# Kernel tuning notes

Hardware: AMD Instinct MI355X
Metric: run time of the kernel (lower is better)

The kernel has to match this reference:

```python
import jax, jax.numpy as jnp
import numpy as np

# dims: episodes E, steps S, comm length L, hidden H, rnn input IN, comm vocab OUT
E, S, L, H, IN, OUT = 64, 32, 32, 1024, 2048, 64
TAU = 2.0      # MTRNN leaky-integrator time constant
EPS = 1e-5     # BatchNorm eps


def setup_inputs() -> dict:
    key = jax.random.key(0)
    ks = jax.random.split(key, 16)
    def p(k, shape, scale=0.02):
        return jax.random.normal(k, shape, jnp.float32) * scale
    return {
        "h_w_action": jax.random.normal(ks[0], (E, S, IN), jnp.float32),
        # MTRNN cell
        "Wx": p(ks[1], (IN, H)), "bx": jnp.zeros((H,), jnp.float32),
        "Wh": p(ks[2], (H, H)), "bh": jnp.zeros((H,), jnp.float32),
        # Ted_Conv1d: 4 branches, kernels 1/3/5/7, each H//4 out channels (OIH layout)
        "w1": p(ks[3], (H // 4, H, 1)), "b1": jnp.zeros((H // 4,), jnp.float32),
        "w3": p(ks[4], (H // 4, H, 3)), "b3": jnp.zeros((H // 4,), jnp.float32),
        "w5": p(ks[5], (H // 4, H, 5)), "b5": jnp.zeros((H // 4,), jnp.float32),
        "w7": p(ks[6], (H // 4, H, 7)), "b7": jnp.zeros((H // 4,), jnp.float32),
        # BatchNorm1d affine
        "gamma": jnp.ones((H,), jnp.float32), "beta": jnp.zeros((H,), jnp.float32),
        # PReLU (single shared slope, torch default init 0.25)
        "prelu_a": jnp.array(0.25, jnp.float32),
        # output Linear
        "Wout": p(ks[7], (H, OUT)), "bout": jnp.zeros((OUT,), jnp.float32),
    }


def _conv(x, w, b):
    # x: [N, C, L], w: [O, I, k], 'same' padding for odd kernels
    pad = (w.shape[-1] - 1) // 2
    y = jax.lax.conv_general_dilated(x, w, (1,), [(pad, pad)],
                                     dimension_numbers=('NCH', 'OIH', 'NCH'))
    return y + b[None, :, None]


def reference(h_w_action, Wx, bx, Wh, bh, w1, b1, w3, b3, w5, b5, w7, b7,
              gamma, beta, prelu_a, Wout, bout):
    # MTRNN: same input every step; leaky integration h' = (1-1/tau)h + (1/tau)tanh(Wx x + Wh h)
    x_r = h_w_action @ Wx + bx                      # [E,S,H], constant across steps
    h0 = jnp.zeros((E, S, H), h_w_action.dtype)

    def step(h, _):
        h_new = (1.0 - 1.0 / TAU) * h + (1.0 / TAU) * jnp.tanh(x_r + h @ Wh + bh)
        return h_new, h_new

    _, hs = jax.lax.scan(step, h0, None, length=L)  # [L,E,S,H]
    hs = hs.transpose(1, 2, 0, 3).reshape(E * S, L, H)

    # multi-kernel conv over the comm-length axis
    xc = hs.transpose(0, 2, 1)                      # [N,H,L]
    y = jnp.concatenate([_conv(xc, w1, b1), _conv(xc, w3, b3),
                         _conv(xc, w5, b5), _conv(xc, w7, b7)], axis=1)  # [N,H,L]

    # BatchNorm1d (training-mode batch stats over N and L), affine
    mean = y.mean(axis=(0, 2), keepdims=True)
    var = y.var(axis=(0, 2), keepdims=True)
    y = (y - mean) * jax.lax.rsqrt(var + EPS) * gamma[None, :, None] + beta[None, :, None]

    # PReLU; Dropout is identity at eval
    y = jnp.where(y > 0, y, prelu_a * y)

    y = y.transpose(0, 2, 1).reshape(E, S, L, H)
    return y @ Wout + bout                          # [E,S,L,OUT]
```

## Files before the change

### kernel.cpp

```cpp
#include <hip/hip_runtime.h>
#include <cstdint>
#include <cmath>

#define DI __device__ __forceinline__


typedef __attribute__((ext_vector_type(8))) short bf16x8;
typedef __attribute__((ext_vector_type(4))) short s16x4;
typedef __attribute__((ext_vector_type(4))) float f32x4;

DI float bf2f(short u){
  union { unsigned int i; float f; } v; v.i = ((unsigned int)(unsigned short)u) << 16; return v.f;
}
DI short f2bf(float f){
  unsigned int x = __builtin_bit_cast(unsigned int, f);
  unsigned int r = (x + 0x7FFFu + ((x >> 16) & 1u)) >> 16;
  return (short)(unsigned short)r;
}
DI void gload16(const void* g, void* l){
  __builtin_amdgcn_global_load_lds(
      (const __attribute__((address_space(1))) unsigned int*)g,
      (__attribute__((address_space(3))) unsigned int*)l, 16, 0, 0);
}

template<int BM, int BN, int MODE>
__global__ __launch_bounds__(256)
void gemm_k(const short* __restrict__ A, long lda,
            const short* __restrict__ Bt, long ldb, int Ksteps,
            const float* __restrict__ bias,
            float* __restrict__ f32out,
            const float* __restrict__ f32in,
            short* __restrict__ bfout, int jj)
{
  constexpr int WTM = BM / 2, WTN = BN / 2;
  constexpr int FM = WTM / 16, FN = WTN / 16;
  constexpr int AIT = BM / 32, BIT = BN / 32;
  __shared__ short As[BM * 64];
  __shared__ short Bs[BN * 64];
  const int tid = threadIdx.x;
  const int w = tid >> 6, l = tid & 63;
  const int wr = w >> 1, wc = w & 1;
  const int lr = l & 15, lk = (l >> 4) << 3;
  const int brow = blockIdx.x * BM;
  const int bcol = blockIdx.y * BN;

  int coff = 0, jout = 0;
  bool first = false;
  if constexpr (MODE == 2) {
    const int bb = bcol >> 7;
    const int dlt = (bb < 2) ? -3 : (bb < 6) ? -2 : (bb < 12) ? -1
                  : (bb < 20) ? 0 : (bb < 26) ? 1 : (bb < 30) ? 2 : 3;
    coff = (dlt == -3) ? 768 : (dlt == -2) ? 256 : (dlt == -1) ? -512
         : (dlt == 0) ? -1536 : (dlt == 1) ? -2304 : (dlt == 2) ? -2816 : -3072;
    jout = jj - dlt;
    if (jout < 0 || jout > 31) return;
    const int ubranch = (bcol + coff) >> 8;
    first = (dlt == -(ubranch < jout ? ubranch : jout));
  }

  f32x4 acc[FM][FN];
  #pragma unroll
  for (int i = 0; i < FM; i++)
    #pragma unroll
    for (int j = 0; j < FN; j++) {
      acc[i][j][0] = 0.f; acc[i][j][1] = 0.f; acc[i][j][2] = 0.f; acc[i][j][3] = 0.f;
    }

  const int rsub = tid >> 3;
  const int koff = (tid & 7) << 3;
  const short* ap[AIT];
  const short* bp[BIT];
  #pragma unroll
  for (int it = 0; it < AIT; ++it)
    ap[it] = A + (long)(brow + it * 32 + rsub) * lda + koff;
  #pragma unroll
  for (int it = 0; it < BIT; ++it)
    bp[it] = Bt + (long)(bcol + it * 32 + rsub) * ldb + koff;

  for (int ks = 0; ks < Ksteps; ++ks) {
    #pragma unroll
    for (int it = 0; it < AIT; ++it) {
      gload16(ap[it], As + ((it * 256 + (w << 6)) << 3));
      ap[it] += 64;
    }
    #pragma unroll
    for (int it = 0; it < BIT; ++it) {
      gload16(bp[it], Bs + ((it * 256 + (w << 6)) << 3));
      bp[it] += 64;
    }
    __syncthreads();
    #pragma unroll
    for (int kk = 0; kk < 64; kk += 32) {
      bf16x8 a[FM], b[FN];
      #pragma unroll
      for (int i = 0; i < FM; i++)
        a[i] = *(const bf16x8*)&As[(wr * WTM + i * 16 + lr) * 64 + kk + lk];
      #pragma unroll
      for (int j = 0; j < FN; j++)
        b[j] = *(const bf16x8*)&Bs[(wc * WTN + j * 16 + lr) * 64 + kk + lk];
      #pragma unroll
      for (int i = 0; i < FM; i++)
        #pragma unroll
        for (int j = 0; j < FN; j++)
          acc[i][j] = __builtin_amdgcn_mfma_f32_16x16x32_bf16(a[i], b[j], acc[i][j], 0, 0, 0);
    }
    __syncthreads();
  }

  const int rbase = brow + wr * WTM;
  const int cbase = bcol + wc * WTN;
  const int rl = (l >> 4) << 2;
  #pragma unroll
  for (int i = 0; i < FM; i++) {
    #pragma unroll
    for (int j = 0; j < FN; j++) {
      #pragma unroll
      for (int r = 0; r < 4; r++) {
        const int row = rbase + i * 16 + rl + r;
        const int col = cbase + j * 16 + lr;
        const float v = acc[i][j][r];
        if constexpr (MODE == 0) {
          f32out[(long)row * 1024 + col] = v + bias[col];
        } else if constexpr (MODE == 1) {
          const long idx = (long)row * 1024 + col;
          const float hp = bf2f(A[(long)row * lda + col]);
          const float hn = 0.5f * hp + 0.5f * tanhf(f32in[idx] + v + bias[col]);
          bfout[idx] = f2bf(hn);
        } else if constexpr (MODE == 2) {
          short* yp = bfout + ((long)row * 32 + jout) * 1024 + (col + coff);
          if (first) *yp = f2bf(v);
          else       *yp = f2bf(bf2f(*yp) + v);
        }
      }
    }
  }
}

__global__ __launch_bounds__(256)
void g5_bn(const short* __restrict__ y, const short* __restrict__ WoutT,
           const float* __restrict__ scal, const float* __restrict__ shft,
           const float* __restrict__ aP, const float* __restrict__ bout,
           float* __restrict__ out)
{
  __shared__ short As[128 * 64];
  __shared__ short Bs[64 * 64];
  __shared__ float sS[1024], sB[1024];
  const int tid = threadIdx.x;
  const int w = tid >> 6, l = tid & 63;
  const int wr = w >> 1, wc = w & 1;
  const int lr = l & 15, lk = (l >> 4) << 3;
  const int m0 = blockIdx.x * 128;
  for (int i = tid; i < 1024; i += 256) { sS[i] = scal[i]; sB[i] = shft[i]; }
  const float a = *aP;
  __syncthreads();

  f32x4 acc[4][2];
  #pragma unroll
  for (int i = 0; i < 4; i++)
    #pragma unroll
    for (int j = 0; j < 2; j++) {
      acc[i][j][0] = 0.f; acc[i][j][1] = 0.f; acc[i][j][2] = 0.f; acc[i][j][3] = 0.f;
    }

  const int rsub = tid >> 3;
  const int koff = (tid & 7) << 3;
  const short* yp[4];
  #pragma unroll
  for (int it = 0; it < 4; ++it)
    yp[it] = y + (long)(m0 + it * 32 + rsub) * 1024 + koff;
  const short* bp[2];
  #pragma unroll
  for (int it = 0; it < 2; ++it)
    bp[it] = WoutT + (long)(it * 32 + rsub) * 1024 + koff;

  for (int ks = 0; ks < 16; ++ks) {
    #pragma unroll
    for (int it = 0; it < 2; ++it) {
      gload16(bp[it], Bs + ((it * 256 + (w << 6)) << 3));
      bp[it] += 64;
    }
    const int c0 = ks * 64 + koff;
    #pragma unroll
    for (int it = 0; it < 4; ++it) {
      bf16x8 v = *(const bf16x8*)yp[it];
      yp[it] += 64;
      #pragma unroll
      for (int e = 0; e < 8; ++e) {
        float f = bf2f(v[e]) * sS[c0 + e] + sB[c0 + e];
        v[e] = f2bf(f > 0.f ? f : a * f);
      }
      *(bf16x8*)(As + ((it * 256 + tid) << 3)) = v;
    }
    __syncthreads();
    #pragma unroll
    for (int kk = 0; kk < 64; kk += 32) {
      bf16x8 af[4], bf_[2];
      #pragma unroll
      for (int i = 0; i < 4; i++)
        af[i] = *(const bf16x8*)&As[(wr * 64 + i * 16 + lr) * 64 + kk + lk];
      #pragma unroll
      for (int j = 0; j < 2; j++)
        bf_[j] = *(const bf16x8*)&Bs[(wc * 32 + j * 16 + lr) * 64 + kk + lk];
      #pragma unroll
      for (int i = 0; i < 4; i++)
        #pragma unroll
        for (int j = 0; j < 2; j++)
          acc[i][j] = __builtin_amdgcn_mfma_f32_16x16x32_bf16(af[i], bf_[j], acc[i][j], 0, 0, 0);
    }
    __syncthreads();
  }

  const int rbase = m0 + wr * 64, cbase = wc * 32;
  const int rl = (l >> 4) << 2;
  #pragma unroll
  for (int i = 0; i < 4; i++)
    #pragma unroll
    for (int j = 0; j < 2; j++)
      #pragma unroll
      for (int r = 0; r < 4; r++) {
        const int row = rbase + i * 16 + rl + r;
        const int col = cbase + j * 16 + lr;
        out[(long)row * 64 + col] = acc[i][j][r] + bout[col];
      }
}

__global__ void zero16(float4* __restrict__ p, long n)
{
  long i = (long)blockIdx.x * 256 + threadIdx.x;
  if (i < n) p[i] = float4{0.f, 0.f, 0.f, 0.f};
}

__global__ void cvt4_f32_bf16(const float* __restrict__ in, short* __restrict__ out, int n4)
{
  int i = blockIdx.x * 256 + threadIdx.x;
  if (i >= n4) return;
  float4 v = ((const float4*)in)[i];
  s16x4 o; o[0] = f2bf(v.x); o[1] = f2bf(v.y); o[2] = f2bf(v.z); o[3] = f2bf(v.w);
  ((s16x4*)out)[i] = o;
}

__global__ void transpose_f32_bf16(const float* __restrict__ in, short* __restrict__ out,
                                   int R, int C)
{
  __shared__ short tile[32][33];
  const int tx = threadIdx.x & 31, ty = threadIdx.x >> 5;
  const int c0 = blockIdx.x * 32, r0 = blockIdx.y * 32;
  #pragma unroll
  for (int i = 0; i < 32; i += 8)
    tile[ty + i][tx] = f2bf(in[(long)(r0 + ty + i) * C + (c0 + tx)]);
  __syncthreads();
  #pragma unroll
  for (int i = 0; i < 32; i += 8)
    out[(long)(c0 + ty + i) * R + (r0 + tx)] = tile[tx][ty + i];
}

__global__ void build_wpack(const float* __restrict__ w1, const float* __restrict__ w3,
                            const float* __restrict__ w5, const float* __restrict__ w7,
                            short* __restrict__ Wp)
{
  const int pc = blockIdx.x;
  int dlt, c;
  if      (pc < 256)  { dlt = -3; c = pc + 768; }
  else if (pc < 768)  { dlt = -2; c = pc + 256; }
  else if (pc < 1536) { dlt = -1; c = pc - 512; }
  else if (pc < 2560) { dlt = 0;  c = pc - 1536; }
  else if (pc < 3328) { dlt = 1;  c = pc - 2304; }
  else if (pc < 3840) { dlt = 2;  c = pc - 2816; }
  else                { dlt = 3;  c = pc - 3072; }
  const int b = c >> 8, kb = 2 * b + 1, t = dlt + b, oo = c & 255;
  const float* w = (b == 0) ? w1 : (b == 1) ? w3 : (b == 2) ? w5 : w7;
  short* dst = Wp + (long)pc * 1024;
  for (int i = threadIdx.x; i < 1024; i += 256)
    dst[i] = f2bf(w[((long)oo * 1024 + i) * kb + t]);
}

__global__ void bn_stats1(const short* __restrict__ y, float* __restrict__ psum,
                          float* __restrict__ pssq)
{
  const int c0 = threadIdx.x * 4;
  float s0 = 0, s1 = 0, s2 = 0, s3 = 0, q0 = 0, q1 = 0, q2 = 0, q3 = 0;
  const long base = (long)blockIdx.x * 64;
  for (int r = 0; r < 64; ++r) {
    s16x4 v = *(const s16x4*)(y + (base + r) * 1024 + c0);
    float f0 = bf2f(v[0]), f1 = bf2f(v[1]), f2v = bf2f(v[2]), f3 = bf2f(v[3]);
    s0 += f0; s1 += f1; s2 += f2v; s3 += f3;
    q0 += f0 * f0; q1 += f1 * f1; q2 += f2v * f2v; q3 += f3 * f3;
  }
  ((float4*)(psum + (long)blockIdx.x * 1024))[threadIdx.x] = float4{s0, s1, s2, s3};
  ((float4*)(pssq + (long)blockIdx.x * 1024))[threadIdx.x] = float4{q0, q1, q2, q3};
}

__global__ __launch_bounds__(256)
void bn_stats2(const float* __restrict__ psum, const float* __restrict__ pssq,
               const float* __restrict__ gamma, const float* __restrict__ beta,
               float* __restrict__ scale, float* __restrict__ shift)
{
  __shared__ float reds[256], redq[256];
  const int ch = threadIdx.x & 7;
  const int rseg = threadIdx.x >> 3;
  const int c = blockIdx.x * 8 + ch;
  float s = 0.f, q = 0.f;
  #pragma unroll 4
  for (int k = 0; k < 32; ++k) {
    const long row = rseg + 32 * k;
    s += psum[row * 1024 + c];
    q += pssq[row * 1024 + c];
  }
  reds[rseg * 8 + ch] = s;
  redq[rseg * 8 + ch] = q;
  __syncthreads();
  #pragma unroll
  for (int st = 16; st > 0; st >>= 1) {
    if (rseg < st) {
      reds[rseg * 8 + ch] += reds[(rseg + st) * 8 + ch];
      redq[rseg * 8 + ch] += redq[(rseg + st) * 8 + ch];
    }
    __syncthreads();
  }
  if (rseg == 0) {
    const float inv = 1.f / 65536.f;
    float mean = reds[ch] * inv;
    float var = redq[ch] * inv - mean * mean;
    float sc = gamma[c] * rsqrtf(var + 1e-5f);
    scale[c] = sc;
    shift[c] = beta[c] - mean * sc;
  }
}

extern "C" void kernel_launch(void* const* d_in, const int* in_sizes, int n_in,
                              void* d_out, int out_size, void* d_ws, size_t ws_size,
                              hipStream_t stream)
{
  const float* h_w_action = (const float*)d_in[0];
  const float* Wx   = (const float*)d_in[1];
  const float* bx   = (const float*)d_in[2];
  const float* Wh   = (const float*)d_in[3];
  const float* bh   = (const float*)d_in[4];
  const float* w1   = (const float*)d_in[5];
  const float* w3   = (const float*)d_in[7];
  const float* w5   = (const float*)d_in[9];
  const float* w7   = (const float*)d_in[11];
  const float* gamma = (const float*)d_in[13];
  const float* beta  = (const float*)d_in[14];
  const float* prelu = (const float*)d_in[15];
  const float* Wout  = (const float*)d_in[16];
  const float* bout  = (const float*)d_in[17];
  float* out = (float*)d_out;

  char* p = (char*)d_ws;
  auto alloc = [&](size_t bytes) -> char* {
    char* r = p; p += (bytes + 255) & ~(size_t)255; return r;
  };
  short* y     = (short*)alloc(65536L * 1024 * 2);
  float* xr    = (float*)alloc(2048L * 1024 * 4);
  float* psum  = (float*)alloc(1024L * 1024 * 4);
  float* pssq  = (float*)alloc(1024L * 1024 * 4);
  short* hb0   = (short*)alloc(2048L * 1024 * 2);
  short* hb1   = (short*)alloc(2048L * 1024 * 2);
  short* A1    = (short*)alloc(2048L * 2048 * 2);
  short* WxT   = (short*)alloc(1024L * 2048 * 2);
  short* WhT   = (short*)alloc(1024L * 1024 * 2);
  short* Wp    = (short*)alloc(4096L * 1024 * 2);
  short* WoutT = (short*)alloc(64L * 1024 * 2);
  float* scal  = (float*)alloc(1024 * 4);
  float* shft  = (float*)alloc(1024 * 4);

  if ((size_t)(p - (char*)d_ws) > ws_size) return;

  zero16<<<1024, 256, 0, stream>>>((float4*)hb0, 2048L * 1024 * 2 / 16);

  cvt4_f32_bf16<<<4096, 256, 0, stream>>>(h_w_action, A1, 2048 * 2048 / 4);
  transpose_f32_bf16<<<dim3(32, 64), 256, 0, stream>>>(Wx, WxT, 2048, 1024);
  transpose_f32_bf16<<<dim3(32, 32), 256, 0, stream>>>(Wh, WhT, 1024, 1024);
  transpose_f32_bf16<<<dim3(2, 32), 256, 0, stream>>>(Wout, WoutT, 1024, 64);
  build_wpack<<<4096, 256, 0, stream>>>(w1, w3, w5, w7, Wp);

  gemm_k<64, 64, 0><<<dim3(32, 16), 256, 0, stream>>>(
      A1, 2048, WxT, 2048, 32, bx, xr, nullptr, nullptr, 0);

  short* hb[2] = {hb0, hb1};
  for (int s = 1; s <= 32; ++s) {
    gemm_k<64, 64, 1><<<dim3(32, 16), 256, 0, stream>>>(
        hb[(s - 1) & 1], 1024, WhT, 1024, 16, bh, nullptr, xr, hb[s & 1], 0);
    gemm_k<128, 128, 2><<<dim3(16, 32), 256, 0, stream>>>(
        hb[s & 1], 1024, Wp, 1024, 16, nullptr, nullptr, nullptr, y, s - 1);
  }

  bn_stats1<<<1024, 256, 0, stream>>>(y, psum, pssq);
  bn_stats2<<<128, 256, 0, stream>>>(psum, pssq, gamma, beta, scal, shft);

  g5_bn<<<dim3(512, 1), 256, 0, stream>>>(y, WoutT, scal, shft, prelu, bout, out);
}
```

Before: 2.046 ms.

## Store recurrent states in padded buffer and run conv as one batched GEMM

The RNN steps now write each hidden state straight into a zero-padded per-sequence buffer (38 slots). The 32 per-step scatter/accumulate conv GEMMs are replaced by a single large GEMM after the recurrence. That GEMM reads shifted windows of the padded states and loops only over the taps each 256-column branch needs. This removes 32 small launches and the read-modify-write bf16 accumulation into y, in exchange for a larger workspace and a workspace-size-dependent fallback path.

```diff
diff --git a/kernel.cpp b/kernel.cpp
--- a/kernel.cpp
+++ b/kernel.cpp
@@ -30,7 +30,7 @@
             const float* __restrict__ bias,
             float* __restrict__ f32out,
             const float* __restrict__ f32in,
-            short* __restrict__ bfout, int jj)
+            short* __restrict__ bfout, long ldout, int jj)
 {
   constexpr int WTM = BM / 2, WTN = BN / 2;
   constexpr int FM = WTM / 16, FN = WTN / 16;
@@ -41,8 +41,8 @@
   const int w = tid >> 6, l = tid & 63;
   const int wr = w >> 1, wc = w & 1;
   const int lr = l & 15, lk = (l >> 4) << 3;
-  const int brow = blockIdx.x * BM;
-  const int bcol = blockIdx.y * BN;
+  const int brow = (MODE == 4) ? blockIdx.y * BM : blockIdx.x * BM;
+  const int bcol = (MODE == 4) ? blockIdx.x * BN : blockIdx.y * BN;
 
   int coff = 0, jout = 0;
   bool first = false;
@@ -68,27 +68,8 @@
 
   const int rsub = tid >> 3;
   const int koff = (tid & 7) << 3;
-  const short* ap[AIT];
-  const short* bp[BIT];
-  #pragma unroll
-  for (int it = 0; it < AIT; ++it)
-    ap[it] = A + (long)(brow + it * 32 + rsub) * lda + koff;
-  #pragma unroll
-  for (int it = 0; it < BIT; ++it)
-    bp[it] = Bt + (long)(bcol + it * 32 + rsub) * ldb + koff;
-
-  for (int ks = 0; ks < Ksteps; ++ks) {
-    #pragma unroll
-    for (int it = 0; it < AIT; ++it) {
-      gload16(ap[it], As + ((it * 256 + (w << 6)) << 3));
-      ap[it] += 64;
-    }
-    #pragma unroll
-    for (int it = 0; it < BIT; ++it) {
-      gload16(bp[it], Bs + ((it * 256 + (w << 6)) << 3));
-      bp[it] += 64;
-    }
-    __syncthreads();
+
+  auto compute = [&]() {
     #pragma unroll
     for (int kk = 0; kk < 64; kk += 32) {
       bf16x8 a[FM], b[FN];
@@ -104,7 +85,62 @@
         for (int j = 0; j < FN; j++)
           acc[i][j] = __builtin_amdgcn_mfma_f32_16x16x32_bf16(a[i], b[j], acc[i][j], 0, 0, 0);
     }
-    __syncthreads();
+  };
+
+  if constexpr (MODE == 4) {
+    const int b = bcol >> 8;
+    const int d0 = 3 - b, d1 = 3 + b;
+    const short* ap[AIT];
+    #pragma unroll
+    for (int it = 0; it < AIT; ++it) {
+      const int m = brow + it * 32 + rsub;
+      ap[it] = A + ((long)(m >> 5) * 38 + (m & 31) + d0) * 1024 + koff;
+    }
+    for (int d = d0; d <= d1; ++d) {
+      const short* bp[BIT];
+      #pragma unroll
+      for (int it = 0; it < BIT; ++it)
+        bp[it] = Bt + (long)(d * 1024 + bcol + it * 32 + rsub) * 1024 + koff;
+      for (int ks = 0; ks < 16; ++ks) {
+        #pragma unroll
+        for (int it = 0; it < AIT; ++it) {
+          gload16(ap[it], As + ((it * 256 + (w << 6)) << 3));
+          ap[it] += 64;
+        }
+        #pragma unroll
+        for (int it = 0; it < BIT; ++it) {
+          gload16(bp[it], Bs + ((it * 256 + (w << 6)) << 3));
+          bp[it] += 64;
+        }
+        __syncthreads();
+        compute();
+        __syncthreads();
+      }
+    }
+  } else {
+    const short* ap[AIT];
+    const short* bp[BIT];
+    #pragma unroll
+    for (int it = 0; it < AIT; ++it)
+      ap[it] = A + (long)(brow + it * 32 + rsub) * lda + koff;
+    #pragma unroll
+    for (int it = 0; it < BIT; ++it)
+      bp[it] = Bt + (long)(bcol + it * 32 + rsub) * ldb + koff;
+    for (int ks = 0; ks < Ksteps; ++ks) {
+      #pragma unroll
+      for (int it = 0; it < AIT; ++it) {
+        gload16(ap[it], As + ((it * 256 + (w << 6)) << 3));
+        ap[it] += 64;
+      }
+      #pragma unroll
+      for (int it = 0; it < BIT; ++it) {
+        gload16(bp[it], Bs + ((it * 256 + (w << 6)) << 3));
+        bp[it] += 64;
+      }
+      __syncthreads();
+      compute();
+      __syncthreads();
+    }
   }
 
   const int rbase = brow + wr * WTM;
@@ -122,14 +158,15 @@
         if constexpr (MODE == 0) {
           f32out[(long)row * 1024 + col] = v + bias[col];
         } else if constexpr (MODE == 1) {
-          const long idx = (long)row * 1024 + col;
           const float hp = bf2f(A[(long)row * lda + col]);
-          const float hn = 0.5f * hp + 0.5f * tanhf(f32in[idx] + v + bias[col]);
-          bfout[idx] = f2bf(hn);
+          const float hn = 0.5f * hp + 0.5f * tanhf(f32in[(long)row * 1024 + col] + v + bias[col]);
+          bfout[(long)row * ldout + col] = f2bf(hn);
         } else if constexpr (MODE == 2) {
           short* yp = bfout + ((long)row * 32 + jout) * 1024 + (col + coff);
           if (first) *yp = f2bf(v);
           else       *yp = f2bf(bf2f(*yp) + v);
+        } else if constexpr (MODE == 4) {
+          bfout[(long)row * 1024 + col] = f2bf(v);
         }
       }
     }
@@ -230,6 +267,16 @@
   if (i < n) p[i] = float4{0.f, 0.f, 0.f, 0.f};
 }
 
+__global__ void zpad(short* __restrict__ hsPad)
+{
+  long i = (long)blockIdx.x * 256 + threadIdx.x;
+  const long n = i / (6 * 128);
+  const int rem = (int)(i % (6 * 128));
+  const int sl = rem >> 7, c16 = rem & 127;
+  const int slot = sl < 3 ? sl : sl + 32;
+  ((float4*)(hsPad + (n * 38 + slot) * 1024))[c16] = float4{0.f, 0.f, 0.f, 0.f};
+}
+
 __global__ void cvt4_f32_bf16(const float* __restrict__ in, short* __restrict__ out, int n4)
 {
   int i = blockIdx.x * 256 + threadIdx.x;
@@ -252,6 +299,23 @@
   #pragma unroll
   for (int i = 0; i < 32; i += 8)
     out[(long)(c0 + ty + i) * R + (r0 + tx)] = tile[tx][ty + i];
+}
+
+__global__ void build_convw(const float* __restrict__ w1, const float* __restrict__ w3,
+                            const float* __restrict__ w5, const float* __restrict__ w7,
+                            short* __restrict__ WtT)
+{
+  const int doid = blockIdx.x;
+  const int d = doid >> 10, o = doid & 1023;
+  const int b = o >> 8, k = 2 * b + 1, t = d - 3 + b, oo = o & 255;
+  const float* w = (b == 0) ? w1 : (b == 1) ? w3 : (b == 2) ? w5 : w7;
+  short* dst = WtT + (long)doid * 1024;
+  if (t < 0 || t >= k) {
+    for (int i = threadIdx.x; i < 1024; i += 256) dst[i] = 0;
+  } else {
+    for (int i = threadIdx.x; i < 1024; i += 256)
+      dst[i] = f2bf(w[((long)oo * 1024 + i) * k + t]);
+  }
 }
 
 __global__ void build_wpack(const float* __restrict__ w1, const float* __restrict__ w3,
@@ -347,47 +411,96 @@
   const float* bout  = (const float*)d_in[17];
   float* out = (float*)d_out;
 
+  const size_t A_need = (65536L * 1024 * 2)
+                      + (2048L * 38 * 1024 * 2)
+                      + (7L * 1024 * 1024 * 2)
+                      + (2048L * 1024 * 4)
+                      + (1024L * 1024 * 2)
+                      + (64L * 1024 * 2)
+                      + 2 * 4096 + 4096;
+
   char* p = (char*)d_ws;
   auto alloc = [&](size_t bytes) -> char* {
     char* r = p; p += (bytes + 255) & ~(size_t)255; return r;
   };
-  short* y     = (short*)alloc(65536L * 1024 * 2);
-  float* xr    = (float*)alloc(2048L * 1024 * 4);
-  float* psum  = (float*)alloc(1024L * 1024 * 4);
-  float* pssq  = (float*)alloc(1024L * 1024 * 4);
-  short* hb0   = (short*)alloc(2048L * 1024 * 2);
-  short* hb1   = (short*)alloc(2048L * 1024 * 2);
-  short* A1    = (short*)alloc(2048L * 2048 * 2);
-  short* WxT   = (short*)alloc(1024L * 2048 * 2);
-  short* WhT   = (short*)alloc(1024L * 1024 * 2);
-  short* Wp    = (short*)alloc(4096L * 1024 * 2);
-  short* WoutT = (short*)alloc(64L * 1024 * 2);
-  float* scal  = (float*)alloc(1024 * 4);
-  float* shft  = (float*)alloc(1024 * 4);
-
-  if ((size_t)(p - (char*)d_ws) > ws_size) return;
-
-  zero16<<<1024, 256, 0, stream>>>((float4*)hb0, 2048L * 1024 * 2 / 16);
-
-  cvt4_f32_bf16<<<4096, 256, 0, stream>>>(h_w_action, A1, 2048 * 2048 / 4);
-  transpose_f32_bf16<<<dim3(32, 64), 256, 0, stream>>>(Wx, WxT, 2048, 1024);
-  transpose_f32_bf16<<<dim3(32, 32), 256, 0, stream>>>(Wh, WhT, 1024, 1024);
-  transpose_f32_bf16<<<dim3(2, 32), 256, 0, stream>>>(Wout, WoutT, 1024, 64);
-  build_wpack<<<4096, 256, 0, stream>>>(w1, w3, w5, w7, Wp);
-
-  gemm_k<64, 64, 0><<<dim3(32, 16), 256, 0, stream>>>(
-      A1, 2048, WxT, 2048, 32, bx, xr, nullptr, nullptr, 0);
-
-  short* hb[2] = {hb0, hb1};
-  for (int s = 1; s <= 32; ++s) {
-    gemm_k<64, 64, 1><<<dim3(32, 16), 256, 0, stream>>>(
-        hb[(s - 1) & 1], 1024, WhT, 1024, 16, bh, nullptr, xr, hb[s & 1], 0);
-    gemm_k<128, 128, 2><<<dim3(16, 32), 256, 0, stream>>>(
-        hb[s & 1], 1024, Wp, 1024, 16, nullptr, nullptr, nullptr, y, s - 1);
-  }
-
-  bn_stats1<<<1024, 256, 0, stream>>>(y, psum, pssq);
-  bn_stats2<<<128, 256, 0, stream>>>(psum, pssq, gamma, beta, scal, shft);
-
-  g5_bn<<<dim3(512, 1), 256, 0, stream>>>(y, WoutT, scal, shft, prelu, bout, out);
-}
+
+  if (ws_size >= A_need) {
+    short* y     = (short*)alloc(65536L * 1024 * 2);
+    short* hsPad = (short*)alloc(2048L * 38 * 1024 * 2);
+    char*  slotA = alloc(7L * 1024 * 1024 * 2);
+    short* A1    = (short*)slotA;
+    short* WxT   = (short*)(slotA + 8388608);
+    short* WtT   = (short*)slotA;
+    char*  xrb   = alloc(2048L * 1024 * 4);
+    float* xr    = (float*)xrb;
+    float* psum  = (float*)xrb;
+    float* pssq  = (float*)(xrb + 4194304);
+    short* WhT   = (short*)alloc(1024L * 1024 * 2);
+    short* WoutT = (short*)alloc(64L * 1024 * 2);
+    float* scal  = (float*)alloc(4096);
+    float* shft  = (float*)alloc(4096);
+
+    zpad<<<6144, 256, 0, stream>>>(hsPad);
+
+    cvt4_f32_bf16<<<4096, 256, 0, stream>>>(h_w_action, A1, 2048 * 2048 / 4);
+    transpose_f32_bf16<<<dim3(32, 64), 256, 0, stream>>>(Wx, WxT, 2048, 1024);
+    transpose_f32_bf16<<<dim3(32, 32), 256, 0, stream>>>(Wh, WhT, 1024, 1024);
+    transpose_f32_bf16<<<dim3(2, 32), 256, 0, stream>>>(Wout, WoutT, 1024, 64);
+
+    gemm_k<64, 64, 0><<<dim3(32, 16), 256, 0, stream>>>(
+        A1, 2048, WxT, 2048, 32, bx, xr, nullptr, nullptr, 0, 0);
+
+    build_convw<<<7168, 256, 0, stream>>>(w1, w3, w5, w7, WtT);
+
+    for (int s = 1; s <= 32; ++s) {
+      gemm_k<64, 64, 1><<<dim3(32, 16), 256, 0, stream>>>(
+          hsPad + (long)(s + 1) * 1024, 38L * 1024, WhT, 1024, 16,
+          bh, nullptr, xr, hsPad + (long)(s + 2) * 1024, 38L * 1024, 0);
+    }
+
+    gemm_k<128, 128, 4><<<dim3(8, 512), 256, 0, stream>>>(
+        hsPad, 0, WtT, 0, 16, nullptr, nullptr, nullptr, y, 1024, 0);
+
+    bn_stats1<<<1024, 256, 0, stream>>>(y, psum, pssq);
+    bn_stats2<<<128, 256, 0, stream>>>(psum, pssq, gamma, beta, scal, shft);
+
+    g5_bn<<<dim3(512, 1), 256, 0, stream>>>(y, WoutT, scal, shft, prelu, bout, out);
+  } else {
+    short* y     = (short*)alloc(65536L * 1024 * 2);
+    float* xr    = (float*)alloc(2048L * 1024 * 4);
+    float* psum  = (float*)alloc(1024L * 1024 * 4);
+    float* pssq  = (float*)alloc(1024L * 1024 * 4);
+    short* hb0   = (short*)alloc(2048L * 1024 * 2);
+    short* hb1   = (short*)alloc(2048L * 1024 * 2);
+    short* A1    = (short*)alloc(2048L * 2048 * 2);
+    short* WxT   = (short*)alloc(1024L * 2048 * 2);
+    short* WhT   = (short*)alloc(1024L * 1024 * 2);
+    short* Wp    = (short*)alloc(4096L * 1024 * 2);
+    short* WoutT = (short*)alloc(64L * 1024 * 2);
+    float* scal  = (float*)alloc(4096);
+    float* shft  = (float*)alloc(4096);
+    if ((size_t)(p - (char*)d_ws) > ws_size) return;
+
+    zero16<<<1024, 256, 0, stream>>>((float4*)hb0, 2048L * 1024 * 2 / 16);
+    cvt4_f32_bf16<<<4096, 256, 0, stream>>>(h_w_action, A1, 2048 * 2048 / 4);
+    transpose_f32_bf16<<<dim3(32, 64), 256, 0, stream>>>(Wx, WxT, 2048, 1024);
+    transpose_f32_bf16<<<dim3(32, 32), 256, 0, stream>>>(Wh, WhT, 1024, 1024);
+    transpose_f32_bf16<<<dim3(2, 32), 256, 0, stream>>>(Wout, WoutT, 1024, 64);
+    build_wpack<<<4096, 256, 0, stream>>>(w1, w3, w5, w7, Wp);
+
+    gemm_k<64, 64, 0><<<dim3(32, 16), 256, 0, stream>>>(
+        A1, 2048, WxT, 2048, 32, bx, xr, nullptr, nullptr, 0, 0);
+
+    short* hb[2] = {hb0, hb1};
+    for (int s = 1; s <= 32; ++s) {
+      gemm_k<64, 64, 1><<<dim3(32, 16), 256, 0, stream>>>(
+          hb[(s - 1) & 1], 1024, WhT, 1024, 16, bh, nullptr, xr, hb[s & 1], 1024, 0);
+      gemm_k<128, 128, 2><<<dim3(16, 32), 256, 0, stream>>>(
+          hb[s & 1], 1024, Wp, 1024, 16, nullptr, nullptr, nullptr, y, 0, s - 1);
+    }
+
+    bn_stats1<<<1024, 256, 0, stream>>>(y, psum, pssq);
+    bn_stats2<<<128, 256, 0, stream>>>(psum, pssq, gamma, beta, scal, shft);
+    g5_bn<<<dim3(512, 1), 256, 0, stream>>>(y, WoutT, scal, shft, prelu, bout, out);
+  }
+}
```

New measurement: 2.046 ms. Within noise of the previous version (+0.0%).
